# Performance work log

Hardware: AMD Instinct MI355X
Metric: run time of the kernel (lower is better)

The kernel has to match this reference:

```python
import jax, jax.numpy as jnp
import numpy as np

EPS_COMBINE = float(np.finfo(float).eps)  # combined[combined == 0] = np.finfo(float).eps
LOSS_COEF = 0.01


def cv_squared(v):
    # torch .var() is unbiased -> ddof=1
    return jnp.var(v, ddof=1) / (jnp.mean(v) ** 2 + 1e-10)


def setup_inputs() -> dict:
    key = jax.random.key(0)
    k1, k2, k3, k4 = jax.random.split(key, 4)
    B, D, E, C = 4096, 1024, 8, 4096
    x = jax.random.normal(k1, (B, D), jnp.float32)
    # small scale so exp(expert_out) in combine() stays finite
    w_gate = jax.random.normal(k2, (D, E), jnp.float32) * 0.02
    w_exp = jax.random.normal(k3, (E, D, C), jnp.float32) * 0.02
    b_exp = jax.random.normal(k4, (E, C), jnp.float32) * 0.02
    return {"x": x, "w_gate": w_gate, "w_exp": w_exp, "b_exp": b_exp, "k": 4}


def reference(x, w_gate, w_exp, b_exp, k):
    B, D = x.shape
    E = w_gate.shape[1]
    # --- noisy_top_k_gating with noisy_gating=False ---
    logits = x @ w_gate                                   # [B, E]
    top_logits, top_idx = jax.lax.top_k(logits, min(k + 1, E))
    topk_logits = top_logits[:, :k]
    topk_idx = top_idx[:, :k]
    topk_gates = jax.nn.softmax(topk_logits, axis=1)      # softmax over top-k only
    gates = jnp.zeros((B, E), x.dtype).at[jnp.arange(B)[:, None], topk_idx].set(topk_gates)
    importance = gates.sum(0)
    load = (gates > 0).sum(0).astype(jnp.float32)         # _gates_to_load
    loss = (cv_squared(importance) + cv_squared(load)) * LOSS_COEF
    # --- dispatch + per-expert forward + weighted combine ---
    # Experts with gate==0 contribute exactly 0 to the combine, so the dense
    # einsum over all experts computes the same math as SparseDispatcher.
    expert_out = jnp.einsum('bd,edc->bec', x, w_exp) + b_exp   # [B, E, C]
    combined = jnp.einsum('bec,be->bc', jnp.exp(expert_out), gates)  # weighted scatter-combine
    combined = jnp.where(combined == 0, EPS_COMBINE, combined)
    y = jnp.log(combined)
    return y, loss
```

## Files before the change

### kernel.cpp

```cpp
#include <hip/hip_runtime.h>
#include <stdint.h>

#define B_ROWS 4096
#define D_DIM  1024
#define E_NUM  8
#define C_DIM  4096
#define LOSS_COEF 0.01f
#define EPS_COMBINE 2.220446049250313e-16f

typedef float  f32x4  __attribute__((ext_vector_type(4)));
typedef __bf16 bf16x8 __attribute__((ext_vector_type(8)));

static __device__ __forceinline__ unsigned short f2bf(float f) {
    unsigned int u = __float_as_uint(f);
    u += 0x7fffu + ((u >> 16) & 1u);
    return (unsigned short)(u >> 16);
}

static __device__ __forceinline__ void async16(const void* g, void* l) {
    __builtin_amdgcn_global_load_lds(
        (const __attribute__((address_space(1))) unsigned int*)g,
        (__attribute__((address_space(3))) unsigned int*)l, 16, 0, 0);
}

__global__ void zero_stats_kernel(float* __restrict__ stats) {
    if (threadIdx.x < 16) stats[threadIdx.x] = 0.0f;
}

__global__ __launch_bounds__(256) void transpose_wexp_kernel(
    const float* __restrict__ wexp, unsigned short* __restrict__ wT) {
    __shared__ float T[64][68];
    const int e  = blockIdx.z;
    const int k0 = blockIdx.y * 64;
    const int c0 = blockIdx.x * 64;
    const int t  = threadIdx.x;
    const float* src = wexp + ((size_t)e * D_DIM + k0) * C_DIM + c0;
    #pragma unroll
    for (int i = 0; i < 4; ++i) {
        int kr = i * 16 + (t >> 4);
        int cg = (t & 15) * 4;
        float4 v = *(const float4*)(src + (size_t)kr * C_DIM + cg);
        *(float4*)&T[kr][cg] = v;
    }
    __syncthreads();
    const int cl  = t & 63;
    const int k16 = (t >> 6) * 16;
    unsigned short h[16];
    #pragma unroll
    for (int j = 0; j < 16; ++j) h[j] = f2bf(T[k16 + j][cl]);
    unsigned short* dst = wT + ((size_t)(e * C_DIM + c0 + cl)) * D_DIM + k0 + k16;
    *(uint4*)dst       = ((const uint4*)h)[0];
    *(uint4*)(dst + 8) = ((const uint4*)h)[1];
}

__global__ __launch_bounds__(256) void gating_kernel(
    const float* __restrict__ x,
    const float* __restrict__ wg,
    unsigned short* __restrict__ xb,
    float* __restrict__ gates,
    float* __restrict__ stats) {
    __shared__ float simp[E_NUM], sload[E_NUM];
    const int tid = threadIdx.x;
    if (tid < E_NUM) { simp[tid] = 0.0f; sload[tid] = 0.0f; }
    __syncthreads();
    const int lane = tid & 63;
    const int wid  = tid >> 6;
    const int row  = blockIdx.x * 4 + wid;

    float acc[8] = {0.f,0.f,0.f,0.f,0.f,0.f,0.f,0.f};
    #pragma unroll
    for (int i = 0; i < 4; ++i) {
        int d = i * 256 + lane * 4;
        float4 xv = *(const float4*)(x + (size_t)row * D_DIM + d);
        unsigned short hh[4] = { f2bf(xv.x), f2bf(xv.y), f2bf(xv.z), f2bf(xv.w) };
        *(uint2*)(xb + (size_t)row * D_DIM + d) = *(const uint2*)hh;
        float xa[4] = { xv.x, xv.y, xv.z, xv.w };
        #pragma unroll
        for (int j = 0; j < 4; ++j) {
            const float4* wp = (const float4*)(wg + (size_t)(d + j) * 8);
            float4 w0 = wp[0], w1 = wp[1];
            acc[0] += xa[j] * w0.x; acc[1] += xa[j] * w0.y;
            acc[2] += xa[j] * w0.z; acc[3] += xa[j] * w0.w;
            acc[4] += xa[j] * w1.x; acc[5] += xa[j] * w1.y;
            acc[6] += xa[j] * w1.z; acc[7] += xa[j] * w1.w;
        }
    }
    #pragma unroll
    for (int off = 32; off > 0; off >>= 1)
        #pragma unroll
        for (int e = 0; e < 8; ++e)
            acc[e] += __shfl_xor(acc[e], off, 64);
    if (lane == 0) {
        float val[4]; int idx[4]; unsigned used = 0;
        #pragma unroll
        for (int j = 0; j < 4; ++j) {
            float best = -1e30f; int bi = 0;
            for (int ee = 0; ee < 8; ++ee)
                if (!(used & (1u << ee)) && acc[ee] > best) { best = acc[ee]; bi = ee; }
            used |= 1u << bi; val[j] = best; idx[j] = bi;
        }
        float mx = val[0], sum = 0.f, gv[4];
        #pragma unroll
        for (int j = 0; j < 4; ++j) { gv[j] = __expf(val[j] - mx); sum += gv[j]; }
        float inv = 1.0f / sum;
        float gout[8] = {0.f,0.f,0.f,0.f,0.f,0.f,0.f,0.f};
        #pragma unroll
        for (int j = 0; j < 4; ++j) gout[idx[j]] = gv[j] * inv;
        #pragma unroll
        for (int e = 0; e < 8; ++e) gates[(size_t)row * 8 + e] = gout[e];
        #pragma unroll
        for (int j = 0; j < 4; ++j) {
            atomicAdd(&simp[idx[j]], gv[j] * inv);
            atomicAdd(&sload[idx[j]], 1.0f);
        }
    }
    __syncthreads();
    if (tid < E_NUM) {
        atomicAdd(&stats[tid],          simp[tid]);
        atomicAdd(&stats[E_NUM + tid],  sload[tid]);
    }
}

__global__ void loss_kernel(const float* __restrict__ stats, float* __restrict__ out_loss) {
    if (threadIdx.x == 0) {
        float mi = 0.f, ml = 0.f;
        for (int e = 0; e < 8; ++e) { mi += stats[e]; ml += stats[8 + e]; }
        mi *= 0.125f; ml *= 0.125f;
        float vi = 0.f, vl = 0.f;
        for (int e = 0; e < 8; ++e) {
            float a = stats[e] - mi;     vi += a * a;
            float b = stats[8 + e] - ml; vl += b * b;
        }
        vi *= (1.0f / 7.0f); vl *= (1.0f / 7.0f);
        out_loss[0] = (vi / (mi * mi + 1e-10f) + vl / (ml * ml + 1e-10f)) * LOSS_COEF;
    }
}

__global__ __launch_bounds__(512, 4) void moe_main_kernel(
    const unsigned short* __restrict__ xb,
    const unsigned short* __restrict__ wT,
    const float* __restrict__ bexp,
    const float* __restrict__ gates,
    float* __restrict__ out)
{
    __shared__ unsigned short As[128 * 32];
    __shared__ unsigned short Bs[128 * 32];
    __shared__ float gs[128 * 9];
    __shared__ float bs[8 * 128];

    const int tid  = threadIdx.x;
    const int lane = tid & 63;
    const int wid  = tid >> 6;
    const int wm   = wid >> 2;
    const int wn   = wid & 3;
    const int q    = lane >> 4;
    const int ln   = lane & 15;
    const int row0 = blockIdx.x * 128;
    const int col0 = blockIdx.y * 128;

    for (int i = tid; i < 1024; i += 512)
        gs[(i >> 3) * 9 + (i & 7)] = gates[(size_t)row0 * 8 + i];
    {
        int e = tid >> 6, c2 = (tid & 63) * 2;
        *(float2*)(bs + e * 128 + c2) = *(const float2*)(bexp + (size_t)e * C_DIM + col0 + c2);
    }

    const f32x4 vzero = {0.f, 0.f, 0.f, 0.f};
    f32x4 comb[4][2];
    #pragma unroll
    for (int i = 0; i < 4; ++i)
        #pragma unroll
        for (int j = 0; j < 2; ++j) comb[i][j] = vzero;

    const int rS = tid >> 2;
    const int qg = (tid & 3) ^ (rS & 3);
    const unsigned short* gA  = xb + (size_t)(row0 + rS) * D_DIM + qg * 8;
    const unsigned short* gBb = wT + (size_t)(col0 + rS) * D_DIM + qg * 8;
    char* ldsA = (char*)As + wid * 1024;
    char* ldsB = (char*)Bs + wid * 1024;

    const int fq = ((q ^ (ln & 3)) << 3);

    for (int e = 0; e < E_NUM; ++e) {
        f32x4 acc[4][2];
        #pragma unroll
        for (int i = 0; i < 4; ++i)
            #pragma unroll
            for (int j = 0; j < 2; ++j) acc[i][j] = vzero;

        const unsigned short* gB = gBb + (size_t)e * C_DIM * D_DIM;

        for (int kt = 0; kt < D_DIM / 32; ++kt) {
            async16(gA + kt * 32, ldsA);
            async16(gB + kt * 32, ldsB);

            __syncthreads();

            bf16x8 af[4], bfr[2];
            #pragma unroll
            for (int fm = 0; fm < 4; ++fm)
                af[fm] = *(const bf16x8*)(As + (wm * 64 + fm * 16 + ln) * 32 + fq);
            #pragma unroll
            for (int fn = 0; fn < 2; ++fn)
                bfr[fn] = *(const bf16x8*)(Bs + (wn * 32 + fn * 16 + ln) * 32 + fq);
            #pragma unroll
            for (int fm = 0; fm < 4; ++fm)
                #pragma unroll
                for (int fn = 0; fn < 2; ++fn)
                    acc[fm][fn] = __builtin_amdgcn_mfma_f32_16x16x32_bf16(
                        af[fm], bfr[fn], acc[fm][fn], 0, 0, 0);

            __syncthreads();
        }

        #pragma unroll
        for (int fn = 0; fn < 2; ++fn) {
            float bval = bs[e * 128 + wn * 32 + fn * 16 + ln];
            #pragma unroll
            for (int fm = 0; fm < 4; ++fm)
                #pragma unroll
                for (int r = 0; r < 4; ++r) {
                    float g = gs[(wm * 64 + fm * 16 + q * 4 + r) * 9 + e];
                    comb[fm][fn][r] += g * __expf(acc[fm][fn][r] + bval);
                }
        }
    }

    #pragma unroll
    for (int fm = 0; fm < 4; ++fm)
        #pragma unroll
        for (int fn = 0; fn < 2; ++fn)
            #pragma unroll
            for (int r = 0; r < 4; ++r) {
                int row = row0 + wm * 64 + fm * 16 + q * 4 + r;
                int col = col0 + wn * 32 + fn * 16 + ln;
                float c = comb[fm][fn][r];
                c = (c == 0.0f) ? EPS_COMBINE : c;
                out[(size_t)row * C_DIM + col] = __logf(c);
            }
}

extern "C" void kernel_launch(void* const* d_in, const int* in_sizes, int n_in,
                              void* d_out, int out_size, void* d_ws, size_t ws_size,
                              hipStream_t stream) {
    const float* x    = (const float*)d_in[0];
    const float* wg   = (const float*)d_in[1];
    const float* wexp = (const float*)d_in[2];
    const float* bexp = (const float*)d_in[3];
    float* out = (float*)d_out;
    char*  ws  = (char*)d_ws;

    unsigned short* wT    = (unsigned short*)ws;
    unsigned short* xb    = (unsigned short*)(ws + 67108864);
    float*          gates = (float*)(ws + 75497472);
    float*          stats = (float*)(ws + 75628544);

    zero_stats_kernel<<<1, 64, 0, stream>>>(stats);
    {
        dim3 tg(C_DIM / 64, D_DIM / 64, E_NUM);
        transpose_wexp_kernel<<<tg, 256, 0, stream>>>(wexp, wT);
    }
    gating_kernel<<<B_ROWS / 4, 256, 0, stream>>>(x, wg, xb, gates, stats);
    loss_kernel<<<1, 64, 0, stream>>>(stats, out + (size_t)B_ROWS * C_DIM);

    dim3 grid(B_ROWS / 128, C_DIM / 128);
    moe_main_kernel<<<grid, 512, 0, stream>>>(xb, wT, bexp, gates, out);
}
```

Measured before the change: 612.8 us.

## Process two experts per K-loop with 64-column tiles and coalesce transpose stores

The main MoE GEMM kernel now uses 256-thread blocks covering 128 rows by 64 columns. Each K iteration loads B tiles for two experts at once, so every A fragment read from LDS feeds twice as many MFMAs and the K loop runs half as many times per tile. This halves the __syncthreads count per unit of work. The cost is higher accumulator register pressure and more blocks. The weight transpose kernel also stages bf16 results in a second LDS buffer so its global stores are contiguous 16-byte row writes instead of scattered ones.

```diff
diff --git a/kernel.cpp b/kernel.cpp
--- a/kernel.cpp
+++ b/kernel.cpp
@@ -30,6 +30,7 @@
 __global__ __launch_bounds__(256) void transpose_wexp_kernel(
     const float* __restrict__ wexp, unsigned short* __restrict__ wT) {
     __shared__ float T[64][68];
+    __shared__ unsigned short W[64][72];
     const int e  = blockIdx.z;
     const int k0 = blockIdx.y * 64;
     const int c0 = blockIdx.x * 64;
@@ -39,18 +40,27 @@
     for (int i = 0; i < 4; ++i) {
         int kr = i * 16 + (t >> 4);
         int cg = (t & 15) * 4;
-        float4 v = *(const float4*)(src + (size_t)kr * C_DIM + cg);
-        *(float4*)&T[kr][cg] = v;
-    }
-    __syncthreads();
-    const int cl  = t & 63;
-    const int k16 = (t >> 6) * 16;
-    unsigned short h[16];
-    #pragma unroll
-    for (int j = 0; j < 16; ++j) h[j] = f2bf(T[k16 + j][cl]);
-    unsigned short* dst = wT + ((size_t)(e * C_DIM + c0 + cl)) * D_DIM + k0 + k16;
-    *(uint4*)dst       = ((const uint4*)h)[0];
-    *(uint4*)(dst + 8) = ((const uint4*)h)[1];
+        *(float4*)&T[kr][cg] = *(const float4*)(src + (size_t)kr * C_DIM + cg);
+    }
+    __syncthreads();
+    {
+        const int c  = t & 63;
+        const int kq = (t >> 6) * 16;
+        unsigned short h[16];
+        #pragma unroll
+        for (int j = 0; j < 16; ++j) h[j] = f2bf(T[kq + j][c]);
+        *(uint4*)&W[c][kq]     = ((const uint4*)h)[0];
+        *(uint4*)&W[c][kq + 8] = ((const uint4*)h)[1];
+    }
+    __syncthreads();
+    unsigned short* dstb = wT + (size_t)e * C_DIM * D_DIM;
+    #pragma unroll
+    for (int r = 0; r < 2; ++r) {
+        int i  = r * 256 + t;
+        int c3 = i >> 3;
+        int k8 = (i & 7) * 8;
+        *(uint4*)(dstb + (size_t)(c0 + c3) * D_DIM + k0 + k8) = *(const uint4*)&W[c3][k8];
+    }
 }
 
 __global__ __launch_bounds__(256) void gating_kernel(
@@ -136,7 +146,7 @@
     }
 }
 
-__global__ __launch_bounds__(512, 4) void moe_main_kernel(
+__global__ __launch_bounds__(256, 3) void moe_main_kernel(
     const unsigned short* __restrict__ xb,
     const unsigned short* __restrict__ wT,
     const float* __restrict__ bexp,
@@ -144,25 +154,29 @@
     float* __restrict__ out)
 {
     __shared__ unsigned short As[128 * 32];
-    __shared__ unsigned short Bs[128 * 32];
+    __shared__ unsigned short Bs[2 * 64 * 32];
     __shared__ float gs[128 * 9];
-    __shared__ float bs[8 * 128];
+    __shared__ float bs[8 * 64];
 
     const int tid  = threadIdx.x;
     const int lane = tid & 63;
     const int wid  = tid >> 6;
-    const int wm   = wid >> 2;
-    const int wn   = wid & 3;
+    const int wm   = wid >> 1;
+    const int wn   = wid & 1;
     const int q    = lane >> 4;
     const int ln   = lane & 15;
     const int row0 = blockIdx.x * 128;
-    const int col0 = blockIdx.y * 128;
-
-    for (int i = tid; i < 1024; i += 512)
-        gs[(i >> 3) * 9 + (i & 7)] = gates[(size_t)row0 * 8 + i];
+    const int col0 = blockIdx.y * 64;
+
+    #pragma unroll
+    for (int i = 0; i < 4; ++i) {
+        int idx = i * 256 + tid;
+        gs[(idx >> 3) * 9 + (idx & 7)] = gates[(size_t)row0 * 8 + idx];
+    }
     {
-        int e = tid >> 6, c2 = (tid & 63) * 2;
-        *(float2*)(bs + e * 128 + c2) = *(const float2*)(bexp + (size_t)e * C_DIM + col0 + c2);
+        int e = tid >> 5, c = tid & 31;
+        bs[e * 64 + c]      = bexp[(size_t)e * C_DIM + col0 + c];
+        bs[e * 64 + c + 32] = bexp[(size_t)e * C_DIM + col0 + c + 32];
     }
 
     const f32x4 vzero = {0.f, 0.f, 0.f, 0.f};
@@ -181,48 +195,63 @@
 
     const int fq = ((q ^ (ln & 3)) << 3);
 
-    for (int e = 0; e < E_NUM; ++e) {
-        f32x4 acc[4][2];
+    for (int eg = 0; eg < 4; ++eg) {
+        f32x4 acc[4][2][2];
         #pragma unroll
         for (int i = 0; i < 4; ++i)
             #pragma unroll
-            for (int j = 0; j < 2; ++j) acc[i][j] = vzero;
-
-        const unsigned short* gB = gBb + (size_t)e * C_DIM * D_DIM;
+            for (int j = 0; j < 2; ++j)
+                #pragma unroll
+                for (int e = 0; e < 2; ++e) acc[i][j][e] = vzero;
+
+        const unsigned short* gB0 = gBb + (size_t)(2 * eg)     * C_DIM * D_DIM;
+        const unsigned short* gB1 = gBb + (size_t)(2 * eg + 1) * C_DIM * D_DIM;
 
         for (int kt = 0; kt < D_DIM / 32; ++kt) {
-            async16(gA + kt * 32, ldsA);
-            async16(gB + kt * 32, ldsB);
+            const int ko = kt * 32;
+            async16(gA + ko,               ldsA);
+            async16(gA + ko + 64 * D_DIM,  ldsA + 4096);
+            async16(gB0 + ko,              ldsB);
+            async16(gB1 + ko,              ldsB + 4096);
 
             __syncthreads();
 
-            bf16x8 af[4], bfr[2];
+            bf16x8 af[4], bfr[2][2];
             #pragma unroll
             for (int fm = 0; fm < 4; ++fm)
                 af[fm] = *(const bf16x8*)(As + (wm * 64 + fm * 16 + ln) * 32 + fq);
             #pragma unroll
             for (int fn = 0; fn < 2; ++fn)
-                bfr[fn] = *(const bf16x8*)(Bs + (wn * 32 + fn * 16 + ln) * 32 + fq);
+                #pragma unroll
+                for (int e = 0; e < 2; ++e)
+                    bfr[fn][e] = *(const bf16x8*)(Bs + e * 2048 +
+                                    (wn * 32 + fn * 16 + ln) * 32 + fq);
             #pragma unroll
             for (int fm = 0; fm < 4; ++fm)
                 #pragma unroll
                 for (int fn = 0; fn < 2; ++fn)
-                    acc[fm][fn] = __builtin_amdgcn_mfma_f32_16x16x32_bf16(
-                        af[fm], bfr[fn], acc[fm][fn], 0, 0, 0);
+                    #pragma unroll
+                    for (int e = 0; e < 2; ++e)
+                        acc[fm][fn][e] = __builtin_amdgcn_mfma_f32_16x16x32_bf16(
+                            af[fm], bfr[fn][e], acc[fm][fn][e], 0, 0, 0);
 
             __syncthreads();
         }
 
         #pragma unroll
-        for (int fn = 0; fn < 2; ++fn) {
-            float bval = bs[e * 128 + wn * 32 + fn * 16 + ln];
-            #pragma unroll
-            for (int fm = 0; fm < 4; ++fm)
-                #pragma unroll
-                for (int r = 0; r < 4; ++r) {
-                    float g = gs[(wm * 64 + fm * 16 + q * 4 + r) * 9 + e];
-                    comb[fm][fn][r] += g * __expf(acc[fm][fn][r] + bval);
-                }
+        for (int e = 0; e < 2; ++e) {
+            int eG = eg * 2 + e;
+            #pragma unroll
+            for (int fn = 0; fn < 2; ++fn) {
+                float bval = bs[eG * 64 + wn * 32 + fn * 16 + ln];
+                #pragma unroll
+                for (int fm = 0; fm < 4; ++fm)
+                    #pragma unroll
+                    for (int r = 0; r < 4; ++r) {
+                        float g = gs[(wm * 64 + fm * 16 + q * 4 + r) * 9 + eG];
+                        comb[fm][fn][r] += g * __expf(acc[fm][fn][e][r] + bval);
+                    }
+            }
         }
     }
 
@@ -263,6 +292,6 @@
     gating_kernel<<<B_ROWS / 4, 256, 0, stream>>>(x, wg, xb, gates, stats);
     loss_kernel<<<1, 64, 0, stream>>>(stats, out + (size_t)B_ROWS * C_DIM);
 
-    dim3 grid(B_ROWS / 128, C_DIM / 128);
-    moe_main_kernel<<<grid, 512, 0, stream>>>(xb, wT, bexp, gates, out);
-}
+    dim3 grid(B_ROWS / 128, C_DIM / 64);
+    moe_main_kernel<<<grid, 256, 0, stream>>>(xb, wT, bexp, gates, out);
+}
```

After: 581.8 us. 5.1% less time.
